# Kernel tuning notes

Measured on AMD Instinct MI355X. Metric: run time of the kernel, lower is better.

The kernel has to match this reference:

```python
import jax, jax.numpy as jnp
from jax import lax
import numpy as np

B, S, D, H, O, V = 1024, 128, 256, 2048, 10, 10

def setup_inputs() -> dict:
    key = jax.random.key(0)
    ks = jax.random.split(key, 8)
    x = jax.random.randint(ks[0], (B, S), 0, V)
    embed = jax.random.normal(ks[1], (V, D), dtype=jnp.float32)
    sd_hx = 1.0 / np.sqrt(D)
    sd_hh = 1.0 / np.sqrt(H)
    W_hx = jax.random.uniform(ks[2], (H, D), minval=-sd_hx, maxval=sd_hx)
    b_hx = jax.random.uniform(ks[3], (H,), minval=-sd_hx, maxval=sd_hx)
    W_hh = jax.random.uniform(ks[4], (H, H), minval=-sd_hh, maxval=sd_hh)
    b_hh = jax.random.uniform(ks[5], (H,), minval=-sd_hh, maxval=sd_hh)
    W_oh = jax.random.uniform(ks[6], (O, H), minval=-sd_hh, maxval=sd_hh)
    b_oh = jax.random.uniform(ks[7], (O,), minval=-sd_hh, maxval=sd_hh)
    return {"x": x, "embed": embed, "W_hx": W_hx, "b_hx": b_hx,
            "W_hh": W_hh, "b_hh": b_hh, "W_oh": W_oh, "b_oh": b_oh}

def reference(x, embed, W_hx, b_hx, W_hh, b_hh, W_oh, b_oh):
    e = embed[x]                                   # [B,S,D]
    # precompute input-to-hidden projection for all steps (one big GEMM)
    xh = jnp.einsum('bsd,hd->bsh', e, W_hx) + b_hx  # [B,S,H]
    # step 0: torch code applies ONLY hx (no hh term, no hh bias)
    h0 = jnp.tanh(xh[:, 0])
    def step(h, xt):
        h = jnp.tanh(xt + h @ W_hh.T + b_hh)
        return h, None
    hT, _ = lax.scan(step, h0, jnp.swapaxes(xh[:, 1:], 0, 1))  # scan over time
    o = hT @ W_oh.T + b_oh                         # [B,O]
    return jax.nn.softmax(o, axis=1)               # nn.Softmax() on 2D -> dim=1
```

## Files before the change

kernel.cpp:

```cpp
#include <hip/hip_runtime.h>
#include <stdint.h>
#include <stddef.h>

#define B_ 1024
#define S_ 128
#define D_ 256
#define H_ 2048
#define O_ 10
#define V_ 10

#define BM 128
#define BN 64
#define BK 128
#define NKT (H_ / BK)
#define NSTG 3
#define STG_ELEMS ((BM + BN) * BK)
#define SMEM_BYTES (NSTG * STG_ELEMS * 2)

typedef unsigned short u16;
typedef short v8s __attribute__((ext_vector_type(8)));
typedef float v4f __attribute__((ext_vector_type(4)));
typedef u16 u16x4 __attribute__((ext_vector_type(4)));

__device__ __forceinline__ u16 f2bf(float f) {
  unsigned int u = __float_as_uint(f);
  u += 0x7FFFu + ((u >> 16) & 1u);
  return (u16)(u >> 16);
}
__device__ __forceinline__ float bf2f(u16 h) {
  return __uint_as_float(((unsigned int)h) << 16);
}
__device__ __forceinline__ float fast_tanh(float x) {
  float e = __expf(2.0f * x);
  return 1.0f - 2.0f / (e + 1.0f);
}
__device__ __forceinline__ void gl2lds16(const void* g, void* l) {
  __builtin_amdgcn_global_load_lds(
      (const __attribute__((address_space(1))) uint32_t*)g,
      (__attribute__((address_space(3))) uint32_t*)l, 16, 0, 0);
}

__global__ __launch_bounds__(256) void make_table(const float* __restrict__ embed,
                                                  const float* __restrict__ W_hx,
                                                  const float* __restrict__ b_hx,
                                                  float* __restrict__ Txh) {
  int idx = blockIdx.x * 256 + threadIdx.x;
  int v = idx >> 11, h = idx & 2047;
  const float4* e4 = (const float4*)(embed + v * D_);
  const float4* w4 = (const float4*)(W_hx + (size_t)h * D_);
  float s = b_hx[h];
#pragma unroll 4
  for (int d = 0; d < D_ / 4; ++d) {
    float4 a = e4[d], b = w4[d];
    s = fmaf(a.x, b.x, s); s = fmaf(a.y, b.y, s);
    s = fmaf(a.z, b.z, s); s = fmaf(a.w, b.w, s);
  }
  Txh[idx] = s;
}

__global__ __launch_bounds__(256) void conv_w(const float* __restrict__ W,
                                              u16* __restrict__ Wb) {
  int i = blockIdx.x * 256 + threadIdx.x;
  float4 w = ((const float4*)W)[i];
  u16x4 o = { f2bf(w.x), f2bf(w.y), f2bf(w.z), f2bf(w.w) };
  ((u16x4*)Wb)[i] = o;
}

__global__ __launch_bounds__(256) void init_h0(const float* __restrict__ Txh,
                                               const int* __restrict__ x,
                                               u16* __restrict__ H0) {
  int idx = blockIdx.x * 256 + threadIdx.x;
  int b = idx >> 11, j = idx & 2047;
  int xv = x[b * S_];
  H0[idx] = f2bf(fast_tanh(Txh[xv * H_ + j]));
}


__device__ __forceinline__ void stage_tiles(const u16* __restrict__ Hin,
                                            const u16* __restrict__ Wb,
                                            u16* __restrict__ As, u16* __restrict__ Bs,
                                            int bm, int bn, int kbase, int tid, int w) {
#pragma unroll
  for (int i = 0; i < 4; ++i) {
    int s = i * 512 + tid;
    int m = s >> 4;
    int cg = (s & 15) ^ (m & 15);
    const u16* g = Hin + (size_t)(bm + m) * H_ + kbase + cg * 8;
    u16* lp = As + (size_t)(i * 512 + (w << 6)) * 8;
    gl2lds16(g, lp);
  }
#pragma unroll
  for (int i = 0; i < 2; ++i) {
    int s = i * 512 + tid;
    int n = s >> 4;
    int cg = (s & 15) ^ (n & 15);
    const u16* g = Wb + (size_t)(bn + n) * H_ + kbase + cg * 8;
    u16* lp = Bs + (size_t)(i * 512 + (w << 6)) * 8;
    gl2lds16(g, lp);
  }
}

__global__ __launch_bounds__(512, 2) void rnn_step(const u16* __restrict__ Hin,
                                                   const u16* __restrict__ Wb,
                                                   const float* __restrict__ Txh,
                                                   const int* __restrict__ x,
                                                   const float* __restrict__ b_hh,
                                                   u16* __restrict__ Hout,
                                                   int t) {
  extern __shared__ __align__(16) u16 smem[];

  const int tid = threadIdx.x;
  const int bid = blockIdx.x;
  const int xcd = bid & 7;
  const int sl  = bid >> 3;
  const int xr = xcd >> 2, xc = xcd & 3;
  const int bm = (xr * 4 + (sl >> 3)) * BM;
  const int bn = (xc * 8 + (sl & 7)) * BN;

  const int w = tid >> 6, l = tid & 63;
  const int wr = w >> 1, wc = w & 1;
  const int lane16 = l & 15, quad = l >> 4;

  v4f acc[2][2];
#pragma unroll
  for (int i = 0; i < 2; ++i)
#pragma unroll
    for (int j = 0; j < 2; ++j) acc[i][j] = (v4f){0.f, 0.f, 0.f, 0.f};

  {
    u16* s0 = smem;
    u16* s1 = smem + STG_ELEMS;
    stage_tiles(Hin, Wb, s0, s0 + BM * BK, bm, bn, 0, tid, w);
    stage_tiles(Hin, Wb, s1, s1 + BM * BK, bm, bn, BK, tid, w);
  }

  for (int kt = 0; kt < NKT; ++kt) {
    __builtin_amdgcn_s_barrier();
    asm volatile("" ::: "memory");

    if (kt + 2 < NKT) {
      u16* sb = smem + ((kt + 2) % 3) * STG_ELEMS;
      stage_tiles(Hin, Wb, sb, sb + BM * BK, bm, bn, (kt + 2) * BK, tid, w);
    }

    if (kt < NKT - 2)       asm volatile("s_waitcnt vmcnt(12)" ::: "memory");
    else if (kt == NKT - 2) asm volatile("s_waitcnt vmcnt(6)"  ::: "memory");
    else                    asm volatile("s_waitcnt vmcnt(0)"  ::: "memory");

    __builtin_amdgcn_s_barrier();
    asm volatile("" ::: "memory");

    const u16* Asb = smem + (kt % 3) * STG_ELEMS;
    const u16* Bsb = Asb + BM * BK;

    v8s af[4][2], bf[4][2];
#pragma unroll
    for (int kc = 0; kc < 4; ++kc) {
      const int cc = kc * 4 + quad;
#pragma unroll
      for (int i = 0; i < 2; ++i) {
        int m = wr * 32 + i * 16 + lane16;
        af[kc][i] = *(const v8s*)&Asb[(m * 16 + (cc ^ lane16)) * 8];
      }
#pragma unroll
      for (int j = 0; j < 2; ++j) {
        int n = wc * 32 + j * 16 + lane16;
        bf[kc][j] = *(const v8s*)&Bsb[(n * 16 + (cc ^ lane16)) * 8];
      }
    }
    __builtin_amdgcn_s_setprio(1);
#pragma unroll
    for (int kc = 0; kc < 4; ++kc)
#pragma unroll
      for (int i = 0; i < 2; ++i)
#pragma unroll
        for (int j = 0; j < 2; ++j)
          acc[i][j] = __builtin_amdgcn_mfma_f32_16x16x32_bf16(af[kc][i], bf[kc][j],
                                                              acc[i][j], 0, 0, 0);
    __builtin_amdgcn_s_setprio(0);
  }

  const int colb = bn + wc * 32 + lane16;
  float bh[2];
#pragma unroll
  for (int j = 0; j < 2; ++j) bh[j] = b_hh[colb + j * 16];
#pragma unroll
  for (int i = 0; i < 2; ++i) {
#pragma unroll
    for (int r = 0; r < 4; ++r) {
      int row = bm + wr * 32 + i * 16 + quad * 4 + r;
      const float* trow = Txh + x[row * S_ + t] * H_;
      u16* orow = Hout + (size_t)row * H_;
#pragma unroll
      for (int j = 0; j < 2; ++j) {
        int col = colb + j * 16;
        float v = acc[i][j][r] + trow[col] + bh[j];
        orow[col] = f2bf(fast_tanh(v));
      }
    }
  }
}

__global__ __launch_bounds__(256) void out_softmax(const u16* __restrict__ Hf,
                                                   const float* __restrict__ W_oh,
                                                   const float* __restrict__ b_oh,
                                                   float* __restrict__ out) {
  int b = blockIdx.x, tid = threadIdx.x;
  float hv[8];
  const u16* hr = Hf + (size_t)b * H_ + tid * 8;
#pragma unroll
  for (int u = 0; u < 8; ++u) hv[u] = bf2f(hr[u]);
  float acc[O_];
#pragma unroll
  for (int i = 0; i < O_; ++i) {
    const float* wr = W_oh + (size_t)i * H_ + tid * 8;
    float s = 0.f;
#pragma unroll
    for (int u = 0; u < 8; ++u) s = fmaf(hv[u], wr[u], s);
    acc[i] = s;
  }
#pragma unroll
  for (int off = 32; off > 0; off >>= 1)
#pragma unroll
    for (int i = 0; i < O_; ++i) acc[i] += __shfl_down(acc[i], off);
  __shared__ float red[4][O_];
  if ((tid & 63) == 0)
#pragma unroll
    for (int i = 0; i < O_; ++i) red[tid >> 6][i] = acc[i];
  __syncthreads();
  if (tid == 0) {
    float o[O_], mx = -1e30f;
#pragma unroll
    for (int i = 0; i < O_; ++i) {
      o[i] = red[0][i] + red[1][i] + red[2][i] + red[3][i] + b_oh[i];
      mx = fmaxf(mx, o[i]);
    }
    float se = 0.f;
#pragma unroll
    for (int i = 0; i < O_; ++i) { o[i] = __expf(o[i] - mx); se += o[i]; }
    float inv = 1.f / se;
#pragma unroll
    for (int i = 0; i < O_; ++i) out[b * O_ + i] = o[i] * inv;
  }
}

extern "C" void kernel_launch(void* const* d_in, const int* in_sizes, int n_in,
                              void* d_out, int out_size, void* d_ws, size_t ws_size,
                              hipStream_t stream) {
  const int*   x     = (const int*)  d_in[0];
  const float* embed = (const float*)d_in[1];
  const float* W_hx  = (const float*)d_in[2];
  const float* b_hx  = (const float*)d_in[3];
  const float* W_hh  = (const float*)d_in[4];
  const float* b_hh  = (const float*)d_in[5];
  const float* W_oh  = (const float*)d_in[6];
  const float* b_oh  = (const float*)d_in[7];
  float* out = (float*)d_out;

  static bool attr_set = false;
  if (!attr_set) {
    (void)hipFuncSetAttribute(reinterpret_cast<const void*>(rnn_step),
                              hipFuncAttributeMaxDynamicSharedMemorySize, SMEM_BYTES);
    attr_set = true;
  }

  char* ws = (char*)d_ws;
  float* Txh = (float*)ws;
  u16* Wb = (u16*)(ws + (80 << 10));
  u16* Ha = (u16*)(ws + (80 << 10) + (8 << 20));
  u16* Hb = (u16*)(ws + (80 << 10) + (12 << 20));

  make_table<<<80, 256, 0, stream>>>(embed, W_hx, b_hx, Txh);
  conv_w<<<4096, 256, 0, stream>>>(W_hh, Wb);
  init_h0<<<8192, 256, 0, stream>>>(Txh, x, Ha);

  for (int t = 1; t < S_; ++t) {
    const u16* hin = (t & 1) ? Ha : Hb;
    u16* hout = (t & 1) ? Hb : Ha;
    rnn_step<<<256, 512, SMEM_BYTES, stream>>>(hin, Wb, Txh, x, b_hh, hout, t);
  }
  out_softmax<<<B_, 256, 0, stream>>>(Hb, W_oh, b_oh, out);
}
```

Baseline: 2.275 ms.

## Shrink RNN step blocks to two waves with larger per-wave MFMA tiles

Each block now runs 128 threads (2 waves) instead of 512. Every wave computes a 64x64 output tile with a 4x4 MFMA accumulator grid, and global-to-LDS offsets are precomputed once in registers. LDS fragment loads are double-buffered against MFMA issue inside each k-tile, and the vmcnt thresholds are scaled to match the larger per-thread load count. The aim is more reuse of each fragment and less redundant address math. The cost is higher register pressure and fewer waves per CU to hide memory latency, since the grid stays at 256 blocks.

Measured after the change: 2.945 ms. 1.29x slower.

```diff
diff --git a/kernel.cpp b/kernel.cpp
--- a/kernel.cpp
+++ b/kernel.cpp
@@ -76,31 +76,7 @@
 }
 
 
-__device__ __forceinline__ void stage_tiles(const u16* __restrict__ Hin,
-                                            const u16* __restrict__ Wb,
-                                            u16* __restrict__ As, u16* __restrict__ Bs,
-                                            int bm, int bn, int kbase, int tid, int w) {
-#pragma unroll
-  for (int i = 0; i < 4; ++i) {
-    int s = i * 512 + tid;
-    int m = s >> 4;
-    int cg = (s & 15) ^ (m & 15);
-    const u16* g = Hin + (size_t)(bm + m) * H_ + kbase + cg * 8;
-    u16* lp = As + (size_t)(i * 512 + (w << 6)) * 8;
-    gl2lds16(g, lp);
-  }
-#pragma unroll
-  for (int i = 0; i < 2; ++i) {
-    int s = i * 512 + tid;
-    int n = s >> 4;
-    int cg = (s & 15) ^ (n & 15);
-    const u16* g = Wb + (size_t)(bn + n) * H_ + kbase + cg * 8;
-    u16* lp = Bs + (size_t)(i * 512 + (w << 6)) * 8;
-    gl2lds16(g, lp);
-  }
-}
-
-__global__ __launch_bounds__(512, 2) void rnn_step(const u16* __restrict__ Hin,
+__global__ __launch_bounds__(128, 1) void rnn_step(const u16* __restrict__ Hin,
                                                    const u16* __restrict__ Wb,
                                                    const float* __restrict__ Txh,
                                                    const int* __restrict__ x,
@@ -118,33 +94,53 @@
   const int bn = (xc * 8 + (sl & 7)) * BN;
 
   const int w = tid >> 6, l = tid & 63;
-  const int wr = w >> 1, wc = w & 1;
   const int lane16 = l & 15, quad = l >> 4;
-
-  v4f acc[2][2];
-#pragma unroll
-  for (int i = 0; i < 2; ++i)
-#pragma unroll
-    for (int j = 0; j < 2; ++j) acc[i][j] = (v4f){0.f, 0.f, 0.f, 0.f};
-
-  {
-    u16* s0 = smem;
-    u16* s1 = smem + STG_ELEMS;
-    stage_tiles(Hin, Wb, s0, s0 + BM * BK, bm, bn, 0, tid, w);
-    stage_tiles(Hin, Wb, s1, s1 + BM * BK, bm, bn, BK, tid, w);
-  }
+  const int mbase = w << 6;
+
+  unsigned offA[16], offB[8];
+#pragma unroll
+  for (int i = 0; i < 16; ++i) {
+    int s = i * 128 + tid;
+    int m = s >> 4;
+    int cg = (s & 15) ^ (m & 15);
+    offA[i] = (unsigned)((bm + m) * H_ + cg * 8);
+  }
+#pragma unroll
+  for (int i = 0; i < 8; ++i) {
+    int s = i * 128 + tid;
+    int n = s >> 4;
+    int cg = (s & 15) ^ (n & 15);
+    offB[i] = (unsigned)((bn + n) * H_ + cg * 8);
+  }
+
+#define STAGE(stg, kbase) do {                                              \
+    u16* As_ = smem + (stg) * STG_ELEMS;                                    \
+    u16* Bs_ = As_ + BM * BK;                                               \
+    _Pragma("unroll")                                                       \
+    for (int i_ = 0; i_ < 16; ++i_)                                         \
+      gl2lds16(Hin + offA[i_] + (kbase), As_ + (size_t)(i_ * 128 + mbase) * 8); \
+    _Pragma("unroll")                                                       \
+    for (int i_ = 0; i_ < 8; ++i_)                                          \
+      gl2lds16(Wb + offB[i_] + (kbase), Bs_ + (size_t)(i_ * 128 + mbase) * 8);  \
+  } while (0)
+
+  v4f acc[4][4];
+#pragma unroll
+  for (int i = 0; i < 4; ++i)
+#pragma unroll
+    for (int j = 0; j < 4; ++j) acc[i][j] = (v4f){0.f, 0.f, 0.f, 0.f};
+
+  STAGE(0, 0);
+  STAGE(1, BK);
 
   for (int kt = 0; kt < NKT; ++kt) {
     __builtin_amdgcn_s_barrier();
     asm volatile("" ::: "memory");
 
-    if (kt + 2 < NKT) {
-      u16* sb = smem + ((kt + 2) % 3) * STG_ELEMS;
-      stage_tiles(Hin, Wb, sb, sb + BM * BK, bm, bn, (kt + 2) * BK, tid, w);
-    }
-
-    if (kt < NKT - 2)       asm volatile("s_waitcnt vmcnt(12)" ::: "memory");
-    else if (kt == NKT - 2) asm volatile("s_waitcnt vmcnt(6)"  ::: "memory");
+    if (kt + 2 < NKT) STAGE((kt + 2) % 3, (kt + 2) * BK);
+
+    if (kt < NKT - 2)       asm volatile("s_waitcnt vmcnt(48)" ::: "memory");
+    else if (kt == NKT - 2) asm volatile("s_waitcnt vmcnt(24)" ::: "memory");
     else                    asm volatile("s_waitcnt vmcnt(0)"  ::: "memory");
 
     __builtin_amdgcn_s_barrier();
@@ -153,47 +149,57 @@
     const u16* Asb = smem + (kt % 3) * STG_ELEMS;
     const u16* Bsb = Asb + BM * BK;
 
-    v8s af[4][2], bf[4][2];
-#pragma unroll
-    for (int kc = 0; kc < 4; ++kc) {
-      const int cc = kc * 4 + quad;
-#pragma unroll
-      for (int i = 0; i < 2; ++i) {
-        int m = wr * 32 + i * 16 + lane16;
-        af[kc][i] = *(const v8s*)&Asb[(m * 16 + (cc ^ lane16)) * 8];
-      }
-#pragma unroll
-      for (int j = 0; j < 2; ++j) {
-        int n = wc * 32 + j * 16 + lane16;
-        bf[kc][j] = *(const v8s*)&Bsb[(n * 16 + (cc ^ lane16)) * 8];
-      }
-    }
+    v8s aX[4], bX[4], aY[4], bY[4];
+#define LDSET(AV, BV, kc) do {                                              \
+    const int cc_ = (kc) * 4 + quad;                                        \
+    _Pragma("unroll")                                                       \
+    for (int i_ = 0; i_ < 4; ++i_) {                                        \
+      int m_ = mbase + i_ * 16 + lane16;       \
+      AV[i_] = *(const v8s*)&Asb[(size_t)(m_ * 16 + (cc_ ^ lane16)) * 8];   \
+    }                                                                       \
+    _Pragma("unroll")                                                       \
+    for (int j_ = 0; j_ < 4; ++j_) {                                        \
+      int n_ = j_ * 16 + lane16;                                            \
+      BV[j_] = *(const v8s*)&Bsb[(size_t)(n_ * 16 + (cc_ ^ lane16)) * 8];   \
+    }                                                                       \
+  } while (0)
+#define MM(AV, BV) do {                                                     \
+    _Pragma("unroll")                                                       \
+    for (int i_ = 0; i_ < 4; ++i_)                                          \
+      _Pragma("unroll")                                                     \
+      for (int j_ = 0; j_ < 4; ++j_)                                        \
+        acc[i_][j_] = __builtin_amdgcn_mfma_f32_16x16x32_bf16(              \
+            AV[i_], BV[j_], acc[i_][j_], 0, 0, 0);                          \
+  } while (0)
+
+    LDSET(aX, bX, 0);
+    LDSET(aY, bY, 1);
     __builtin_amdgcn_s_setprio(1);
-#pragma unroll
-    for (int kc = 0; kc < 4; ++kc)
-#pragma unroll
-      for (int i = 0; i < 2; ++i)
-#pragma unroll
-        for (int j = 0; j < 2; ++j)
-          acc[i][j] = __builtin_amdgcn_mfma_f32_16x16x32_bf16(af[kc][i], bf[kc][j],
-                                                              acc[i][j], 0, 0, 0);
+    MM(aX, bX);
+    LDSET(aX, bX, 2);
+    MM(aY, bY);
+    LDSET(aY, bY, 3);
+    MM(aX, bX);
+    MM(aY, bY);
     __builtin_amdgcn_s_setprio(0);
-  }
-
-  const int colb = bn + wc * 32 + lane16;
-  float bh[2];
-#pragma unroll
-  for (int j = 0; j < 2; ++j) bh[j] = b_hh[colb + j * 16];
-#pragma unroll
-  for (int i = 0; i < 2; ++i) {
+#undef LDSET
+#undef MM
+  }
+#undef STAGE
+
+  float bh[4];
+#pragma unroll
+  for (int j = 0; j < 4; ++j) bh[j] = b_hh[bn + j * 16 + lane16];
+#pragma unroll
+  for (int i = 0; i < 4; ++i) {
 #pragma unroll
     for (int r = 0; r < 4; ++r) {
-      int row = bm + wr * 32 + i * 16 + quad * 4 + r;
+      int row = bm + mbase + i * 16 + quad * 4 + r;
       const float* trow = Txh + x[row * S_ + t] * H_;
       u16* orow = Hout + (size_t)row * H_;
 #pragma unroll
-      for (int j = 0; j < 2; ++j) {
-        int col = colb + j * 16;
+      for (int j = 0; j < 4; ++j) {
+        int col = bn + j * 16 + lane16;
         float v = acc[i][j][r] + trow[col] + bh[j];
         orow[col] = f2bf(fast_tanh(v));
       }
@@ -277,7 +283,7 @@
   for (int t = 1; t < S_; ++t) {
     const u16* hin = (t & 1) ? Ha : Hb;
     u16* hout = (t & 1) ? Hb : Ha;
-    rnn_step<<<256, 512, SMEM_BYTES, stream>>>(hin, Wb, Txh, x, b_hh, hout, t);
+    rnn_step<<<256, 128, SMEM_BYTES, stream>>>(hin, Wb, Txh, x, b_hh, hout, t);
   }
   out_softmax<<<B_, 256, 0, stream>>>(Hb, W_oh, b_oh, out);
 }
```
